# Performance work log

Measured on AMD Instinct MI355X. Metric: run time of the kernel, lower is better.

The kernel has to match this reference:

```python
import jax, jax.numpy as jnp
import numpy as np

D_MODEL, N_HEADS, D_FF = 1024, 16, 4096
B, L, PREFIX = 2, 2048, 512
EPS = 1e-5


def _ln(x, w, b):
    mu = jnp.mean(x, axis=-1, keepdims=True)
    var = jnp.mean((x - mu) ** 2, axis=-1, keepdims=True)
    return (x - mu) * jax.lax.rsqrt(var + EPS) * w + b


def setup_inputs() -> dict:
    key = jax.random.key(0)
    ks = jax.random.split(key, 5)
    d, f = D_MODEL, D_FF
    return {
        "x": jax.random.normal(ks[0], (B, L, d), jnp.float32),
        "ln1_w": jnp.ones((d,), jnp.float32),
        "ln1_b": jnp.zeros((d,), jnp.float32),
        "in_proj_w": jax.random.normal(ks[1], (3 * d, d), jnp.float32) / np.sqrt(d),
        "in_proj_b": jnp.zeros((3 * d,), jnp.float32),
        "out_w": jax.random.normal(ks[2], (d, d), jnp.float32) / np.sqrt(d),
        "out_b": jnp.zeros((d,), jnp.float32),
        "ln2_w": jnp.ones((d,), jnp.float32),
        "ln2_b": jnp.zeros((d,), jnp.float32),
        "fc1_w": jax.random.normal(ks[3], (f, d), jnp.float32) / np.sqrt(d),
        "fc1_b": jnp.zeros((f,), jnp.float32),
        "fc2_w": jax.random.normal(ks[4], (d, f), jnp.float32) / np.sqrt(f),
        "fc2_b": jnp.zeros((d,), jnp.float32),
        "prefix_len": PREFIX,
    }


def reference(x, ln1_w, ln1_b, in_proj_w, in_proj_b, out_w, out_b,
              ln2_w, ln2_b, fc1_w, fc1_b, fc2_w, fc2_b, prefix_len):
    Bv, Lv, d = x.shape
    H = N_HEADS
    hd = d // H
    m = prefix_len

    # additive prefix-decoder mask (L, L): allowed if j < m, or (i >= m and j <= i)
    i = jnp.arange(Lv)[:, None]
    j = jnp.arange(Lv)[None, :]
    allowed = (j < m) | ((i >= m) & (j <= i))
    mask = jnp.where(allowed, 0.0, -jnp.inf).astype(x.dtype)

    h = _ln(x, ln1_w, ln1_b)
    qkv = h @ in_proj_w.T + in_proj_b                      # [B, L, 3d]
    q, k, v = jnp.split(qkv, 3, axis=-1)
    q = q.reshape(Bv, Lv, H, hd)
    k = k.reshape(Bv, Lv, H, hd)
    v = v.reshape(Bv, Lv, H, hd)
    scale = 1.0 / np.sqrt(hd)
    scores = jnp.einsum("bihd,bjhd->bhij", q, k) * scale   # [B, H, L, L]
    attn = jax.nn.softmax(scores + mask, axis=-1)
    ctx = jnp.einsum("bhij,bjhd->bihd", attn, v).reshape(Bv, Lv, d)
    sa = ctx @ out_w.T + out_b
    x = x + sa

    h = _ln(x, ln2_w, ln2_b)
    ff = jax.nn.gelu(h @ fc1_w.T + fc1_b, approximate=False) @ fc2_w.T + fc2_b
    return x + ff
```

## Files before the change

### kernel.cpp

```cpp
#include <hip/hip_runtime.h>
#include <cstdint>
#include <cstddef>

#define DM   1024
#define NH   16
#define HD   64
#define DFF  4096
#define BB   2
#define LL   2048
#define MM   (BB*LL)

using short8 = __attribute__((ext_vector_type(8))) short;
using f32x4  = __attribute__((ext_vector_type(4))) float;

__device__ __forceinline__ unsigned short f2bf(float f) {
  union { float f; uint32_t u; } v; v.f = f;
  uint32_t u = v.u;
  uint32_t r = (u + 0x7fffu + ((u >> 16) & 1u)) >> 16;
  return (unsigned short)r;
}

__device__ __forceinline__ uint32_t cvtpk_bf16(float a, float b) {
  uint32_t r;
  asm("v_cvt_pk_bf16_f32 %0, %1, %2" : "=v"(r) : "v"(a), "v"(b));
  return r;
}

__device__ __forceinline__ float exp2_fast(float x) {
  float r;
  asm("v_exp_f32 %0, %1" : "=v"(r) : "v"(x));
  return r;
}

__device__ __forceinline__ float rcp_fast(float x) {
  float r;
  asm("v_rcp_f32 %0, %1" : "=v"(r) : "v"(x));
  return r;
}

__device__ __forceinline__ float gelu_tanh(float v) {
  float y = v * (0.7978845608028654f + 0.035677408136300125f * v * v);
  float e = exp2_fast(y * 2.885390081777927f);
  float tnh = 1.0f - 2.0f * rcp_fast(1.0f + e);
  return 0.5f * v * (1.0f + tnh);
}

#define GLDS16(gp, lp) \
  __builtin_amdgcn_global_load_lds((const __attribute__((address_space(1))) uint32_t*)(gp), \
                                   (__attribute__((address_space(3))) uint32_t*)(lp), 16, 0, 0)

__global__ __launch_bounds__(256) void convert_f32_bf16(const float* __restrict__ in,
                                                        unsigned short* __restrict__ out, int n4) {
  int i = blockIdx.x * 256 + threadIdx.x;
  if (i < n4) {
    float4 v = ((const float4*)in)[i];
    ushort4 o;
    o.x = f2bf(v.x); o.y = f2bf(v.y); o.z = f2bf(v.z); o.w = f2bf(v.w);
    ((ushort4*)out)[i] = o;
  }
}

__global__ __launch_bounds__(256) void ln_kernel(const float* __restrict__ x,
                                                 const float* __restrict__ w,
                                                 const float* __restrict__ b,
                                                 unsigned short* __restrict__ out) {
  int row = blockIdx.x, t = threadIdx.x;
  float4 v = ((const float4*)(x + (size_t)row * DM))[t];
  float s  = v.x + v.y + v.z + v.w;
  float sq = v.x*v.x + v.y*v.y + v.z*v.z + v.w*v.w;
  #pragma unroll
  for (int o = 32; o; o >>= 1) { s += __shfl_down(s, o); sq += __shfl_down(sq, o); }
  __shared__ float sh[8];
  if ((t & 63) == 0) { sh[t >> 6] = s; sh[4 + (t >> 6)] = sq; }
  __syncthreads();
  float S  = sh[0] + sh[1] + sh[2] + sh[3];
  float SQ = sh[4] + sh[5] + sh[6] + sh[7];
  float mu  = S * (1.0f / DM);
  float var = SQ * (1.0f / DM) - mu * mu;
  float rs  = rsqrtf(var + 1e-5f);
  float4 wv = ((const float4*)w)[t];
  float4 bv = ((const float4*)b)[t];
  ushort4 o;
  o.x = f2bf((v.x - mu) * rs * wv.x + bv.x);
  o.y = f2bf((v.y - mu) * rs * wv.y + bv.y);
  o.z = f2bf((v.z - mu) * rs * wv.z + bv.z);
  o.w = f2bf((v.w - mu) * rs * wv.w + bv.w);
  ((ushort4*)(out + (size_t)row * DM))[t] = o;
}

template <int EPI>
__global__ __launch_bounds__(512) void gemm8(const unsigned short* __restrict__ A,
                                             const unsigned short* __restrict__ Bw,
                                             const float* __restrict__ bias,
                                             unsigned short* __restrict__ Cout,
                                             int M, int N, int K, int lda, int ldb) {
  __shared__ unsigned short As[2 * 256 * 64];
  __shared__ unsigned short Bs[2 * 256 * 64];
  const int t = threadIdx.x;
  const int l = t & 63, lr = l & 15, lg = l >> 4;
  const int wid = t >> 6, wm = wid >> 2, wn = wid & 3;

  int bx = blockIdx.x, by = blockIdx.y;
  {
    const int gx = gridDim.x;
    const int total = gx * gridDim.y;
    if ((total & 7) == 0) {
      int lin = by * gx + bx;
      int lin2 = (lin & 7) * (total >> 3) + (lin >> 3);
      bx = lin2 % gx;
      by = lin2 / gx;
    }
  }
  const int m0 = by * 256, n0 = bx * 256;

  f32x4 acc[8][4];
  #pragma unroll
  for (int mi = 0; mi < 8; ++mi)
    #pragma unroll
    for (int ni = 0; ni < 4; ++ni) acc[mi][ni] = {0.f, 0.f, 0.f, 0.f};

  const int rowt = t >> 3, sw = (t & 7) ^ (rowt & 7);
  const unsigned short* Ag = A  + (size_t)(m0 + rowt) * lda + sw * 8;
  const unsigned short* Bg = Bw + (size_t)(n0 + rowt) * ldb + sw * 8;
  const size_t r64A = (size_t)64 * lda;
  const size_t r64B = (size_t)64 * ldb;

  const int rs = lr & 7;
  const int segA = (lg ^ rs) * 8;
  const int segB = ((lg + 4) ^ rs) * 8;

  const int nt = K >> 6;

  auto stage = [&](int kt, int buf) {
    const int k0 = kt << 6;
    char* Ad = (char*)As + buf * 32768 + t * 16;
    char* Bd = (char*)Bs + buf * 32768 + t * 16;
    #pragma unroll
    for (int g = 0; g < 4; ++g) GLDS16(Ag + k0 + g * r64A, Ad + g * 8192);
    #pragma unroll
    for (int g = 0; g < 4; ++g) GLDS16(Bg + k0 + g * r64B, Bd + g * 8192);
  };

  stage(0, 0);
  stage(1, 1);

  for (int kt = 0; kt < nt; ++kt) {
    const int cur = kt & 1;
    if (kt + 1 < nt) {
      asm volatile("s_waitcnt vmcnt(8)" ::: "memory");
    } else {
      asm volatile("s_waitcnt vmcnt(0)" ::: "memory");
    }
    __builtin_amdgcn_s_barrier();
    asm volatile("" ::: "memory");

    const unsigned short* Ab = As + cur * 16384;
    const unsigned short* Bb = Bs + cur * 16384;
    short8 bfr[4][2];
    #pragma unroll
    for (int ni = 0; ni < 4; ++ni) {
      const int row = wn * 64 + ni * 16 + lr;
      bfr[ni][0] = *(const short8*)&Bb[row * 64 + segA];
      bfr[ni][1] = *(const short8*)&Bb[row * 64 + segB];
    }
    __builtin_amdgcn_s_setprio(1);
    #pragma unroll
    for (int mp = 0; mp < 4; ++mp) {
      short8 af[2][2];
      #pragma unroll
      for (int q = 0; q < 2; ++q) {
        const int row = wm * 128 + (mp * 2 + q) * 16 + lr;
        af[q][0] = *(const short8*)&Ab[row * 64 + segA];
        af[q][1] = *(const short8*)&Ab[row * 64 + segB];
      }
      #pragma unroll
      for (int q = 0; q < 2; ++q)
        #pragma unroll
        for (int ni = 0; ni < 4; ++ni) {
          acc[mp * 2 + q][ni] = __builtin_amdgcn_mfma_f32_16x16x32_bf16(af[q][0], bfr[ni][0], acc[mp * 2 + q][ni], 0, 0, 0);
          acc[mp * 2 + q][ni] = __builtin_amdgcn_mfma_f32_16x16x32_bf16(af[q][1], bfr[ni][1], acc[mp * 2 + q][ni], 0, 0, 0);
        }
    }
    __builtin_amdgcn_s_setprio(0);

    asm volatile("" ::: "memory");
    __builtin_amdgcn_s_barrier();
    asm volatile("" ::: "memory");
    if (kt + 2 < nt) stage(kt + 2, cur);
  }

  #pragma unroll
  for (int mi = 0; mi < 8; ++mi) {
    int row = m0 + wm * 128 + mi * 16 + lg * 4;
    #pragma unroll
    for (int ni = 0; ni < 4; ++ni) {
      int col = n0 + wn * 64 + ni * 16 + lr;
      float bv = bias[col];
      #pragma unroll
      for (int r = 0; r < 4; ++r) {
        float v = acc[mi][ni][r] + bv;
        size_t idx = (size_t)(row + r) * N + col;
        if (EPI == 0) {
          Cout[idx] = f2bf(v);
        } else {
          Cout[idx] = f2bf(gelu_tanh(v));
        }
      }
    }
  }
}

template <int EPI, int BM>
__global__ __launch_bounds__(256) void gemm_bt(const unsigned short* __restrict__ A,
                                               const unsigned short* __restrict__ Bw,
                                               const float* __restrict__ bias,
                                               const float* __restrict__ res,
                                               void* __restrict__ Cout,
                                               int M, int N, int K, int lda, int ldb) {
  constexpr int MI   = BM / 32;
  constexpr int ABUF = BM * 64;
  __shared__ unsigned short As[2 * ABUF];
  __shared__ unsigned short Bs[2 * 64 * 64];
  const int t = threadIdx.x;
  const int l = t & 63, lr = l & 15, lg = l >> 4;
  const int w = t >> 6, wm = w >> 1, wn = w & 1;

  int bx = blockIdx.x, by = blockIdx.y;
  {
    const int gx = gridDim.x;
    const int total = gx * gridDim.y;
    if ((total & 7) == 0) {
      int lin = by * gx + bx;
      int lin2 = (lin & 7) * (total >> 3) + (lin >> 3);
      bx = lin2 % gx;
      by = lin2 / gx;
    }
  }
  const int m0 = by * BM, n0 = bx * 64;

  f32x4 acc[MI][2];
  #pragma unroll
  for (int mi = 0; mi < MI; ++mi)
    #pragma unroll
    for (int ni = 0; ni < 2; ++ni) acc[mi][ni] = {0.f, 0.f, 0.f, 0.f};

  const int rowt = t >> 3, sw = (t & 7) ^ (rowt & 7);
  const unsigned short* Ag = A  + (size_t)(m0 + rowt) * lda + sw * 8;
  const unsigned short* Bg = Bw + (size_t)(n0 + rowt) * ldb + sw * 8;
  char* AsB = (char*)As + t * 16;
  char* BsB = (char*)Bs + t * 16;
  const size_t r32A = (size_t)32 * lda;
  const size_t r32B = (size_t)32 * ldb;

  const int rs = lr & 7;
  const int segA = (lg ^ rs) * 8;
  const int segB = ((lg + 4) ^ rs) * 8;

  #pragma unroll
  for (int g = 0; g < MI; ++g) GLDS16(Ag + g * r32A, AsB + g * 4096);
  GLDS16(Bg,        BsB);
  GLDS16(Bg + r32B, BsB + 4096);

  int cur = 0;
  for (int k0 = 0; k0 < K; k0 += 64, cur ^= 1) {
    __syncthreads();
    const int kn = k0 + 64;
    if (kn < K) {
      char* An = AsB + (cur ^ 1) * (ABUF * 2);
      char* Bn = BsB + (cur ^ 1) * 8192;
      #pragma unroll
      for (int g = 0; g < MI; ++g) GLDS16(Ag + kn + g * r32A, An + g * 4096);
      GLDS16(Bg + kn,        Bn);
      GLDS16(Bg + kn + r32B, Bn + 4096);
    }
    const unsigned short* Ab = As + cur * ABUF;
    const unsigned short* Bb = Bs + cur * (64 * 64);
    short8 af[MI][2], bfr[2][2];
    #pragma unroll
    for (int mi = 0; mi < MI; ++mi) {
      const int row = wm * (BM / 2) + mi * 16 + lr;
      af[mi][0] = *(const short8*)&Ab[row * 64 + segA];
      af[mi][1] = *(const short8*)&Ab[row * 64 + segB];
    }
    #pragma unroll
    for (int ni = 0; ni < 2; ++ni) {
      const int row = wn * 32 + ni * 16 + lr;
      bfr[ni][0] = *(const short8*)&Bb[row * 64 + segA];
      bfr[ni][1] = *(const short8*)&Bb[row * 64 + segB];
    }
    #pragma unroll
    for (int mi = 0; mi < MI; ++mi)
      #pragma unroll
      for (int ni = 0; ni < 2; ++ni) {
        acc[mi][ni] = __builtin_amdgcn_mfma_f32_16x16x32_bf16(af[mi][0], bfr[ni][0], acc[mi][ni], 0, 0, 0);
        acc[mi][ni] = __builtin_amdgcn_mfma_f32_16x16x32_bf16(af[mi][1], bfr[ni][1], acc[mi][ni], 0, 0, 0);
      }
  }

  #pragma unroll
  for (int mi = 0; mi < MI; ++mi) {
    int row = m0 + wm * (BM / 2) + mi * 16 + lg * 4;
    #pragma unroll
    for (int ni = 0; ni < 2; ++ni) {
      int col = n0 + wn * 32 + ni * 16 + lr;
      float bv = (EPI == 3) ? 0.f : bias[col];
      #pragma unroll
      for (int r = 0; r < 4; ++r) {
        float v = acc[mi][ni][r] + bv;
        size_t idx = (size_t)(row + r) * N + col;
        if (EPI == 0) {
          ((unsigned short*)Cout)[idx] = f2bf(v);
        } else if (EPI == 1) {
          ((float*)Cout)[idx] = res[idx] + v;
        } else if (EPI == 2) {
          ((unsigned short*)Cout)[idx] = f2bf(gelu_tanh(v));
        } else {
          ((float*)Cout)[idx] += v;
        }
      }
    }
  }
}

__global__ __launch_bounds__(256) void vtrans_kernel(const unsigned short* __restrict__ qkv,
                                                     unsigned short* __restrict__ vt) {
  __shared__ unsigned short tile[64][72];
  int bh = blockIdx.y, b = bh >> 4, h = bh & 15;
  int j0 = blockIdx.x * 64, t = threadIdx.x;
  #pragma unroll
  for (int r = 0; r < 2; ++r) {
    int j = r * 32 + (t >> 3), d0 = (t & 7) * 8;
    short8 v = *(const short8*)(qkv + (size_t)(b * LL + j0 + j) * 3072 + 2048 + h * 64 + d0);
    #pragma unroll
    for (int e = 0; e < 8; ++e) tile[j][d0 + e] = (unsigned short)v[e];
  }
  __syncthreads();
  #pragma unroll
  for (int r = 0; r < 2; ++r) {
    int d = r * 32 + (t >> 3), j = (t & 7) * 8;
    short8 o;
    #pragma unroll
    for (int e = 0; e < 8; ++e) o[e] = (short)tile[j + e][d];
    *(short8*)(vt + (size_t)(bh * 64 + d) * LL + j0 + j) = o;
  }
}

__global__ __launch_bounds__(512) void attn_kernel(const unsigned short* __restrict__ qkv,
                                                   const unsigned short* __restrict__ vt,
                                                   const int* __restrict__ prefix,
                                                   unsigned short* __restrict__ ctx) {
  __shared__ unsigned short Ks[2][64 * 64];
  __shared__ unsigned short Vs[2][64 * 64];
  __shared__ unsigned short Plds[8][16][72];
  const int t = threadIdx.x, w = t >> 6, l = t & 63, lr = l & 15, lg = l >> 4;
  const int bh = blockIdx.y, b = bh >> 4, h = bh & 15;
  const int ib = gridDim.x - 1 - blockIdx.x;
  const int i0 = ib * 128, iw = i0 + w * 16;
  const int m = *prefix;
  const float C = 0.125f * 1.44269504088896f;

  const int r0 = t >> 3, s0 = t & 7, swz = s0 ^ (r0 & 7);
  const unsigned short* Kg0 = qkv + (size_t)(b * LL + r0) * 3072 + DM + h * 64 + swz * 8;
  const unsigned short* Vg0 = vt + (size_t)(bh * 64 + r0) * LL + swz * 8;
  char* KdB = (char*)Ks + t * 16;
  char* VdB = (char*)Vs + t * 16;
  const int rs = lr & 7;
  const int segA = (lg ^ rs) * 8;
  const int segB = ((lg + 4) ^ rs) * 8;

  short8 qf[2];
  {
    const unsigned short* qrow = qkv + (size_t)(b * LL + iw + lr) * 3072 + h * 64;
    qf[0] = *(const short8*)(qrow + lg * 8);
    qf[1] = *(const short8*)(qrow + 32 + lg * 8);
  }
  short8 ones;
  #pragma unroll
  for (int e = 0; e < 8; ++e) ones[e] = (short)0x3F80;

  f32x4 Ot[4];
  #pragma unroll
  for (int dt = 0; dt < 4; ++dt) Ot[dt] = {0.f, 0.f, 0.f, 0.f};
  f32x4 Osum = {0.f, 0.f, 0.f, 0.f};

  const int jmax = (i0 + 128 <= m) ? m : (i0 + 128);
  const int nb = (jmax + 63) >> 6;
  const int i_abs = iw + lr;

  GLDS16(Kg0, KdB);
  GLDS16(Vg0, VdB);

  for (int c = 0; c < nb; ++c) {
    __syncthreads();
    if (c + 1 < nb) {
      const size_t jn = (size_t)(c + 1) * 64;
      const int pn = (c + 1) & 1;
      GLDS16(Kg0 + jn * 3072, KdB + pn * 8192);
      GLDS16(Vg0 + jn,        VdB + pn * 8192);
    }
    const int jt = c * 64, p = c & 1;

    f32x4 sc[4];
    #pragma unroll
    for (int nt = 0; nt < 4; ++nt) {
      sc[nt] = {0.f, 0.f, 0.f, 0.f};
      const int row = nt * 16 + lr;
      short8 kf0 = *(const short8*)&Ks[p][row * 64 + segA];
      short8 kf1 = *(const short8*)&Ks[p][row * 64 + segB];
      sc[nt] = __builtin_amdgcn_mfma_f32_16x16x32_bf16(kf0, qf[0], sc[nt], 0, 0, 0);
      sc[nt] = __builtin_amdgcn_mfma_f32_16x16x32_bf16(kf1, qf[1], sc[nt], 0, 0, 0);
    }
    const bool full = (jt + 64 <= m) || (iw >= m && jt + 64 <= iw + 1);
    #pragma unroll
    for (int nt = 0; nt < 4; ++nt) {
      float p0 = exp2_fast(sc[nt][0] * C);
      float p1 = exp2_fast(sc[nt][1] * C);
      float p2 = exp2_fast(sc[nt][2] * C);
      float p3 = exp2_fast(sc[nt][3] * C);
      if (!full) {
        const int jb = jt + nt * 16 + lg * 4;
        const bool causal_i = (i_abs >= m);
        p0 = ((jb + 0 < m) || (causal_i && jb + 0 <= i_abs)) ? p0 : 0.f;
        p1 = ((jb + 1 < m) || (causal_i && jb + 1 <= i_abs)) ? p1 : 0.f;
        p2 = ((jb + 2 < m) || (causal_i && jb + 2 <= i_abs)) ? p2 : 0.f;
        p3 = ((jb + 3 < m) || (causal_i && jb + 3 <= i_abs)) ? p3 : 0.f;
      }
      uint2 pk;
      pk.x = cvtpk_bf16(p0, p1);
      pk.y = cvtpk_bf16(p2, p3);
      *(uint2*)&Plds[w][lr][nt * 16 + lg * 4] = pk;
    }
    short8 paf0 = *(const short8*)&Plds[w][lr][lg * 8];
    short8 paf1 = *(const short8*)&Plds[w][lr][32 + lg * 8];
    #pragma unroll
    for (int dt = 0; dt < 4; ++dt) {
      const int row = dt * 16 + lr;
      short8 vf0 = *(const short8*)&Vs[p][row * 64 + segA];
      short8 vf1 = *(const short8*)&Vs[p][row * 64 + segB];
      Ot[dt] = __builtin_amdgcn_mfma_f32_16x16x32_bf16(paf0, vf0, Ot[dt], 0, 0, 0);
      Ot[dt] = __builtin_amdgcn_mfma_f32_16x16x32_bf16(paf1, vf1, Ot[dt], 0, 0, 0);
    }
    Osum = __builtin_amdgcn_mfma_f32_16x16x32_bf16(paf0, ones, Osum, 0, 0, 0);
    Osum = __builtin_amdgcn_mfma_f32_16x16x32_bf16(paf1, ones, Osum, 0, 0, 0);
  }
  #pragma unroll
  for (int r = 0; r < 4; ++r) {
    float inv = 1.0f / Osum[r];
    size_t row = (size_t)(b * LL + iw + lg * 4 + r);
    #pragma unroll
    for (int dt = 0; dt < 4; ++dt)
      ctx[row * DM + h * 64 + dt * 16 + lr] = f2bf(Ot[dt][r] * inv);
  }
}

extern "C" void kernel_launch(void* const* d_in, const int* in_sizes, int n_in,
                              void* d_out, int out_size, void* d_ws, size_t ws_size,
                              hipStream_t stream) {
  const float* x        = (const float*)d_in[0];
  const float* ln1_w    = (const float*)d_in[1];
  const float* ln1_b    = (const float*)d_in[2];
  const float* in_proj_w= (const float*)d_in[3];
  const float* in_proj_b= (const float*)d_in[4];
  const float* out_w    = (const float*)d_in[5];
  const float* out_b    = (const float*)d_in[6];
  const float* ln2_w    = (const float*)d_in[7];
  const float* ln2_b    = (const float*)d_in[8];
  const float* fc1_w    = (const float*)d_in[9];
  const float* fc1_b    = (const float*)d_in[10];
  const float* fc2_w    = (const float*)d_in[11];
  const float* fc2_b    = (const float*)d_in[12];
  const int*   prefix   = (const int*)d_in[13];
  float* outp = (float*)d_out;

  char* ws = (char*)d_ws;
  unsigned short* slab  = (unsigned short*)ws;
  float*          x2    = (float*)(ws + ((size_t)8 << 20));
  unsigned short* vtb   = (unsigned short*)(ws + ((size_t)8 << 20));
  unsigned short* wslab = (unsigned short*)(ws + ((size_t)24 << 20));
  unsigned short* qkv   = (unsigned short*)(ws + ((size_t)32 << 20));
  unsigned short* wfc2  = (unsigned short*)(ws + ((size_t)32 << 20));
  unsigned short* ffh   = (unsigned short*)(ws + ((size_t)40 << 20));
  const bool big = ws_size >= ((size_t)72 << 20);

  convert_f32_bf16<<<3072, 256, 0, stream>>>(in_proj_w, wslab, 3072 * 1024 / 4);
  ln_kernel<<<MM, 256, 0, stream>>>(x, ln1_w, ln1_b, slab);
  gemm8<0><<<dim3(3072 / 256, MM / 256), 512, 0, stream>>>(slab, wslab, in_proj_b, qkv, MM, 3072, 1024, 1024, 1024);
  vtrans_kernel<<<dim3(LL / 64, BB * NH), 256, 0, stream>>>(qkv, vtb);
  attn_kernel<<<dim3(LL / 128, BB * NH), 512, 0, stream>>>(qkv, vtb, prefix, slab);
  convert_f32_bf16<<<1024, 256, 0, stream>>>(out_w, wslab, 1024 * 1024 / 4);
  gemm_bt<1, 64><<<dim3(1024 / 64, MM / 64), 256, 0, stream>>>(slab, wslab, out_b, x, x2, MM, 1024, 1024, 1024, 1024);

  ln_kernel<<<MM, 256, 0, stream>>>(x2, ln2_w, ln2_b, slab);
  convert_f32_bf16<<<4096, 256, 0, stream>>>(fc1_w, wslab, 4096 * 1024 / 4);
  convert_f32_bf16<<<4096, 256, 0, stream>>>(fc2_w, wfc2, 1024 * 4096 / 4);
  if (big) {
    unsigned short* ffmid = (unsigned short*)(ws + ((size_t)40 << 20));
    gemm8<2><<<dim3(4096 / 256, MM / 256), 512, 0, stream>>>(slab, wslab, fc1_b, ffmid, MM, 4096, 1024, 1024, 1024);
    gemm_bt<1, 64><<<dim3(1024 / 64, MM / 64), 256, 0, stream>>>(ffmid, wfc2, fc2_b, x2, outp, MM, 1024, 4096, 4096, 4096);
  } else {
    gemm_bt<2, 128><<<dim3(2048 / 64, MM / 128), 256, 0, stream>>>(slab, wslab, fc1_b, nullptr, ffh, MM, 2048, 1024, 1024, 1024);
    gemm_bt<1, 64><<<dim3(1024 / 64, MM / 64), 256, 0, stream>>>(ffh, wfc2, fc2_b, x2, outp, MM, 1024, 2048, 2048, 4096);
    gemm_bt<2, 128><<<dim3(2048 / 64, MM / 128), 256, 0, stream>>>(slab, wslab + (size_t)2048 * 1024, fc1_b + 2048, nullptr, ffh, MM, 2048, 1024, 1024, 1024);
    gemm_bt<3, 64><<<dim3(1024 / 64, MM / 64), 256, 0, stream>>>(ffh, wfc2 + 2048, nullptr, nullptr, outp, MM, 1024, 2048, 2048, 4096);
  }
}
```

Baseline: 229.5 us.

## Split 256x256 GEMM tile into four quadrant phases with staggered half-tile prefetch

Restructures the 256x256 bf16 GEMM main loop so each K step runs four quadrant phases. Each phase computes one 128x128 sub-tile, and the loads of the next K step's A/B halves are issued one half at a time between phases, with finer vmcnt waits. The aim is to keep global-to-LDS traffic spread out and overlapped with MFMA work instead of bursting after a full-tile barrier. In exchange it needs four barriers per K step instead of two, and the next buffer is written while other phases still read, which depends on careful wait ordering.

```diff
diff --git a/kernel.cpp b/kernel.cpp
--- a/kernel.cpp
+++ b/kernel.cpp
@@ -94,11 +94,13 @@
                                              const float* __restrict__ bias,
                                              unsigned short* __restrict__ Cout,
                                              int M, int N, int K, int lda, int ldb) {
-  __shared__ unsigned short As[2 * 256 * 64];
-  __shared__ unsigned short Bs[2 * 256 * 64];
+  __shared__ unsigned short As[2][2][128 * 64];
+  __shared__ unsigned short Bs[2][2][128 * 64];
   const int t = threadIdx.x;
   const int l = t & 63, lr = l & 15, lg = l >> 4;
-  const int wid = t >> 6, wm = wid >> 2, wn = wid & 3;
+  const int wid = t >> 6;
+  const int wr = wid & 3;
+  const int wc = wid >> 2;
 
   int bx = blockIdx.x, by = blockIdx.y;
   {
@@ -113,11 +115,13 @@
   }
   const int m0 = by * 256, n0 = bx * 256;
 
-  f32x4 acc[8][4];
-  #pragma unroll
-  for (int mi = 0; mi < 8; ++mi)
-    #pragma unroll
-    for (int ni = 0; ni < 4; ++ni) acc[mi][ni] = {0.f, 0.f, 0.f, 0.f};
+  f32x4 acc[4][2][4];
+  #pragma unroll
+  for (int q = 0; q < 4; ++q)
+    #pragma unroll
+    for (int fr = 0; fr < 2; ++fr)
+      #pragma unroll
+      for (int fc = 0; fc < 4; ++fc) acc[q][fr][fc] = {0.f, 0.f, 0.f, 0.f};
 
   const int rowt = t >> 3, sw = (t & 7) ^ (rowt & 7);
   const unsigned short* Ag = A  + (size_t)(m0 + rowt) * lda + sw * 8;
@@ -127,83 +131,97 @@
 
   const int rs = lr & 7;
   const int segA = (lg ^ rs) * 8;
-  const int segB = ((lg + 4) ^ rs) * 8;
+  const int segB4 = ((lg + 4) ^ rs) * 8;
 
   const int nt = K >> 6;
 
-  auto stage = [&](int kt, int buf) {
+  auto stageA = [&](int kt, int buf, int h) {
     const int k0 = kt << 6;
-    char* Ad = (char*)As + buf * 32768 + t * 16;
-    char* Bd = (char*)Bs + buf * 32768 + t * 16;
-    #pragma unroll
-    for (int g = 0; g < 4; ++g) GLDS16(Ag + k0 + g * r64A, Ad + g * 8192);
-    #pragma unroll
-    for (int g = 0; g < 4; ++g) GLDS16(Bg + k0 + g * r64B, Bd + g * 8192);
+    char* d = (char*)&As[buf][h][0] + t * 16;
+    const unsigned short* g = Ag + (size_t)(h * 128) * lda + k0;
+    GLDS16(g,        d);
+    GLDS16(g + r64A, d + 8192);
   };
-
-  stage(0, 0);
-  stage(1, 1);
+  auto stageB = [&](int kt, int buf, int h) {
+    const int k0 = kt << 6;
+    char* d = (char*)&Bs[buf][h][0] + t * 16;
+    const unsigned short* g = Bg + (size_t)(h * 128) * ldb + k0;
+    GLDS16(g,        d);
+    GLDS16(g + r64B, d + 8192);
+  };
+
+  stageA(0, 0, 0); stageB(0, 0, 0); stageA(0, 0, 1); stageB(0, 0, 1);
 
   for (int kt = 0; kt < nt; ++kt) {
-    const int cur = kt & 1;
-    if (kt + 1 < nt) {
-      asm volatile("s_waitcnt vmcnt(8)" ::: "memory");
-    } else {
-      asm volatile("s_waitcnt vmcnt(0)" ::: "memory");
-    }
-    __builtin_amdgcn_s_barrier();
-    asm volatile("" ::: "memory");
-
-    const unsigned short* Ab = As + cur * 16384;
-    const unsigned short* Bb = Bs + cur * 16384;
-    short8 bfr[4][2];
-    #pragma unroll
-    for (int ni = 0; ni < 4; ++ni) {
-      const int row = wn * 64 + ni * 16 + lr;
-      bfr[ni][0] = *(const short8*)&Bb[row * 64 + segA];
-      bfr[ni][1] = *(const short8*)&Bb[row * 64 + segB];
-    }
-    __builtin_amdgcn_s_setprio(1);
-    #pragma unroll
-    for (int mp = 0; mp < 4; ++mp) {
+    const int cur = kt & 1, nxt = cur ^ 1;
+    const bool more = (kt + 1 < nt);
+    #pragma unroll
+    for (int q = 0; q < 4; ++q) {
+      if (more) {
+        asm volatile("s_waitcnt vmcnt(4)" ::: "memory");
+      } else {
+        if (q == 0)      asm volatile("s_waitcnt vmcnt(4)" ::: "memory");
+        else if (q == 1) asm volatile("s_waitcnt vmcnt(2)" ::: "memory");
+        else             asm volatile("s_waitcnt vmcnt(0)" ::: "memory");
+      }
+      __builtin_amdgcn_s_barrier();
+      if (more) {
+        if (q == 0)      stageA(kt + 1, nxt, 0);
+        else if (q == 1) stageB(kt + 1, nxt, 0);
+        else if (q == 2) stageA(kt + 1, nxt, 1);
+        else             stageB(kt + 1, nxt, 1);
+      }
+      __builtin_amdgcn_sched_barrier(0);
+      const int ah = (q == 1 || q == 2) ? 1 : 0;
+      const int bh = (q >= 2) ? 1 : 0;
+      const unsigned short* Ab = &As[cur][ah][0];
+      const unsigned short* Bb = &Bs[cur][bh][0];
+      short8 bf[4][2];
+      #pragma unroll
+      for (int fc = 0; fc < 4; ++fc) {
+        const int row = wc * 64 + fc * 16 + lr;
+        bf[fc][0] = *(const short8*)&Bb[row * 64 + segA];
+        bf[fc][1] = *(const short8*)&Bb[row * 64 + segB4];
+      }
       short8 af[2][2];
       #pragma unroll
-      for (int q = 0; q < 2; ++q) {
-        const int row = wm * 128 + (mp * 2 + q) * 16 + lr;
-        af[q][0] = *(const short8*)&Ab[row * 64 + segA];
-        af[q][1] = *(const short8*)&Ab[row * 64 + segB];
-      }
-      #pragma unroll
-      for (int q = 0; q < 2; ++q)
+      for (int fr = 0; fr < 2; ++fr) {
+        const int row = wr * 32 + fr * 16 + lr;
+        af[fr][0] = *(const short8*)&Ab[row * 64 + segA];
+        af[fr][1] = *(const short8*)&Ab[row * 64 + segB4];
+      }
+      __builtin_amdgcn_s_setprio(1);
+      #pragma unroll
+      for (int fr = 0; fr < 2; ++fr)
         #pragma unroll
-        for (int ni = 0; ni < 4; ++ni) {
-          acc[mp * 2 + q][ni] = __builtin_amdgcn_mfma_f32_16x16x32_bf16(af[q][0], bfr[ni][0], acc[mp * 2 + q][ni], 0, 0, 0);
-          acc[mp * 2 + q][ni] = __builtin_amdgcn_mfma_f32_16x16x32_bf16(af[q][1], bfr[ni][1], acc[mp * 2 + q][ni], 0, 0, 0);
+        for (int fc = 0; fc < 4; ++fc) {
+          acc[q][fr][fc] = __builtin_amdgcn_mfma_f32_16x16x32_bf16(af[fr][0], bf[fc][0], acc[q][fr][fc], 0, 0, 0);
+          acc[q][fr][fc] = __builtin_amdgcn_mfma_f32_16x16x32_bf16(af[fr][1], bf[fc][1], acc[q][fr][fc], 0, 0, 0);
         }
-    }
-    __builtin_amdgcn_s_setprio(0);
-
-    asm volatile("" ::: "memory");
-    __builtin_amdgcn_s_barrier();
-    asm volatile("" ::: "memory");
-    if (kt + 2 < nt) stage(kt + 2, cur);
-  }
-
-  #pragma unroll
-  for (int mi = 0; mi < 8; ++mi) {
-    int row = m0 + wm * 128 + mi * 16 + lg * 4;
-    #pragma unroll
-    for (int ni = 0; ni < 4; ++ni) {
-      int col = n0 + wn * 64 + ni * 16 + lr;
-      float bv = bias[col];
-      #pragma unroll
-      for (int r = 0; r < 4; ++r) {
-        float v = acc[mi][ni][r] + bv;
-        size_t idx = (size_t)(row + r) * N + col;
-        if (EPI == 0) {
-          Cout[idx] = f2bf(v);
-        } else {
-          Cout[idx] = f2bf(gelu_tanh(v));
+      __builtin_amdgcn_s_setprio(0);
+    }
+  }
+
+  #pragma unroll
+  for (int q = 0; q < 4; ++q) {
+    const int ah = (q == 1 || q == 2) ? 1 : 0;
+    const int bh = (q >= 2) ? 1 : 0;
+    #pragma unroll
+    for (int fr = 0; fr < 2; ++fr) {
+      int row = m0 + ah * 128 + wr * 32 + fr * 16 + lg * 4;
+      #pragma unroll
+      for (int fc = 0; fc < 4; ++fc) {
+        int col = n0 + bh * 128 + wc * 64 + fc * 16 + lr;
+        float bv = bias[col];
+        #pragma unroll
+        for (int r = 0; r < 4; ++r) {
+          float v = acc[q][fr][fc][r] + bv;
+          size_t idx = (size_t)(row + r) * N + col;
+          if (EPI == 0) {
+            Cout[idx] = f2bf(v);
+          } else {
+            Cout[idx] = f2bf(gelu_tanh(v));
+          }
         }
       }
     }
```

Result: slower. 266.8 us (+16.3%).
